# Kernel optimization log

Measured on AMD Instinct MI355X. Metric: run time of the kernel, lower is better.

Reference implementation:

```python
import jax, jax.numpy as jnp
import numpy as np
import math
from jax import lax

B, C, BINS, W = 2, 8, 1024, 512
HEADS = 8
HD = BINS // HEADS            # 128 head dim
ROT = HD // 2                 # rotary rot_dim = bins//num_heads//2 = 64


def setup_inputs() -> dict:
    key = jax.random.key(0)
    k1, k2, k3, k4, k5 = jax.random.split(key, 5)
    s_lin = 1.0 / math.sqrt(BINS)
    return {
        "x": jax.random.normal(k1, (B, C, BINS, W), dtype=jnp.float32),
        "Wq_lin": jax.random.uniform(k2, (C, BINS, BINS), jnp.float32, -s_lin, s_lin),
        "Wq_conv": jax.random.normal(k3, (C, C, 1, 3), dtype=jnp.float32) * 0.1,
        "bq_conv": jax.random.normal(k4, (C,), dtype=jnp.float32) * 0.1,
        "Wout": jax.random.uniform(k5, (C, BINS, BINS), jnp.float32, -s_lin, s_lin),
    }


def _mc_linear(x, Wc):
    # separable MultichannelLinear: out[b,c,o,w] = sum_i W[c,o,i] x[b,c,i,w]
    return jnp.einsum('coi,bciw->bcow', Wc, x)


def _proj(x, Wl, Wc, bc):
    y = _mc_linear(x, Wl)
    y = lax.conv_general_dilated(y, Wc, (1, 1), ((0, 0), (1, 1)),
                                 dimension_numbers=('NCHW', 'OIHW', 'NCHW'))
    return y + bc[None, :, None, None]


def _to_heads(y):
    # [b,c,bins,w] -> [b,c,H,w,hd]
    b, c, _, w = y.shape
    return y.transpose(0, 1, 3, 2).reshape(b, c, w, HEADS, HD).transpose(0, 1, 3, 2, 4)


def _rotary(t):
    # lucidrains RotaryEmbedding(dim=ROT, freqs_for='lang'): rotate first ROT dims over seq axis (-2)
    inv = 1.0 / (10000.0 ** (jnp.arange(0, ROT, 2, dtype=jnp.float32) / ROT))  # [ROT//2]
    pos = jnp.arange(t.shape[-2], dtype=jnp.float32)
    f = jnp.repeat(pos[:, None] * inv[None, :], 2, axis=-1)  # [w, ROT] interleaved repeat
    cos, sin = jnp.cos(f), jnp.sin(f)
    left, right = t[..., :ROT], t[..., ROT:]
    x1, x2 = left[..., 0::2], left[..., 1::2]
    rot = jnp.stack([-x2, x1], axis=-1).reshape(left.shape)
    return jnp.concatenate([left * cos + rot * sin, right], axis=-1)


def reference(x, Wq_lin, Wq_conv, bq_conv, Wout):
    b, c, h, w = x.shape
    # NOTE: original forward uses q_proj for q, k AND v (k_proj/v_proj unused)
    qp = _proj(x, Wq_lin, Wq_conv, bq_conv)
    qh = _to_heads(qp)                       # [b,c,H,w,hd]
    q = _rotary(qh)
    k = _rotary(qh)
    v = qh
    scale = 1.0 / math.sqrt(h)               # custom scale: sqrt(bins), not sqrt(head_dim)
    qk = jnp.einsum('bchqd,bchkd->bchqk', q, k) * scale
    a = jnp.einsum('bchqk,bchkd->bchqd', jax.nn.softmax(qk, axis=-1), v)
    # [b,c,H,w,hd] -> [b,c,bins,w]
    a = a.transpose(0, 1, 3, 2, 4).reshape(b, c, w, h).transpose(0, 1, 3, 2)
    return _mc_linear(a, Wout)
```

## Files before the change

kernel.cpp:

```cpp
#include <hip/hip_runtime.h>
#include <cstddef>

#define Bb 2
#define Cc_ 8
#define BINS 1024
#define Ww 512
#define HEADS 8
#define HD 128
#define NELEM (Bb*Cc_*BINS*Ww)

typedef __attribute__((ext_vector_type(8)))  __bf16 bf16x8;
typedef __attribute__((ext_vector_type(4)))  __bf16 bf16x4;
typedef __attribute__((ext_vector_type(4)))  float  f32x4;
typedef __attribute__((ext_vector_type(16))) float  f32x16;
#define MFMA32(a,b,c) __builtin_amdgcn_mfma_f32_32x32x16_bf16(a,b,c,0,0,0)

__device__ __forceinline__ void async16(const __bf16* g, __bf16* l) {
    __builtin_amdgcn_global_load_lds(
        (const __attribute__((address_space(1))) void*)g,
        (__attribute__((address_space(3))) void*)l, 16, 0, 0);
}

__global__ void __launch_bounds__(256) cast_bf16_2(const float* __restrict__ inA,
                                                   const float* __restrict__ inB,
                                                   __bf16* __restrict__ outA,
                                                   __bf16* __restrict__ outB) {
    const float* in = blockIdx.y ? inB : inA;
    __bf16* out     = blockIdx.y ? outB : outA;
    size_t i = ((size_t)blockIdx.x * 256 + threadIdx.x) * 8;
    float4 a = *(const float4*)&in[i];
    float4 b = *(const float4*)&in[i + 4];
    bf16x8 o = {(__bf16)a.x, (__bf16)a.y, (__bf16)a.z, (__bf16)a.w,
                (__bf16)b.x, (__bf16)b.y, (__bf16)b.z, (__bf16)b.w};
    *(bf16x8*)&out[i] = o;
}

__global__ void __launch_bounds__(256) transpose_cast_x(const float* __restrict__ x,
                                                        __bf16* __restrict__ xT) {
    int w0 = blockIdx.x * 64, i0 = blockIdx.y * 64, bc = blockIdx.z;
    const float* src = x + (size_t)bc * BINS * Ww;
    __bf16* dst = xT + (size_t)bc * Ww * BINS;
    __shared__ float T[64][65];
    int t = threadIdx.x;
    #pragma unroll
    for (int pass = 0; pass < 4; pass++) {
        int idx = t + pass * 256;
        int il = idx >> 4, ch = idx & 15;
        float4 v = *(const float4*)&src[(size_t)(i0 + il) * Ww + w0 + ch * 4];
        T[il][ch * 4 + 0] = v.x; T[il][ch * 4 + 1] = v.y;
        T[il][ch * 4 + 2] = v.z; T[il][ch * 4 + 3] = v.w;
    }
    __syncthreads();
    #pragma unroll
    for (int pass = 0; pass < 2; pass++) {
        int idx = t + pass * 256;
        int wl = idx >> 3, ch = idx & 7;
        bf16x8 o;
        #pragma unroll
        for (int j = 0; j < 8; j++) o[j] = (__bf16)T[ch * 8 + j][wl];
        *(bf16x8*)&dst[(size_t)(w0 + wl) * BINS + i0 + ch * 8] = o;
    }
}

template<bool BF16OUT>
__global__ void __launch_bounds__(256) gemm32(const __bf16* __restrict__ Wall,
                                              const __bf16* __restrict__ Bt,
                                              void* __restrict__ Yv) {
    int bc = blockIdx.z, c = bc & 7;
    const __bf16* A  = Wall + (size_t)c  * BINS * BINS;
    const __bf16* Bm = Bt   + (size_t)bc * Ww * BINS;
    int n0 = blockIdx.x * 128, m0 = blockIdx.y * 128;

    __shared__ __bf16 Asm[128 * 32];
    __shared__ __bf16 Bsm[128 * 32];

    int t = threadIdx.x, w = t >> 6, l = t & 63;
    int l31 = l & 31, h = l >> 5;
    int wm = w >> 1, wn = w & 1;

    int rowS[2], colS[2];
    #pragma unroll
    for (int j = 0; j < 2; j++) {
        int p = (w * 2 + j) * 64 + l;
        int r = p >> 2, cs = (p & 3) ^ (r & 3);
        rowS[j] = r; colS[j] = cs * 8;
    }

    f32x16 acc[2][2];
    #pragma unroll
    for (int a = 0; a < 2; a++)
        #pragma unroll
        for (int b = 0; b < 2; b++)
            #pragma unroll
            for (int r = 0; r < 16; r++) acc[a][b][r] = 0.f;

    for (int k0 = 0; k0 < BINS; k0 += 32) {
        __syncthreads();
        #pragma unroll
        for (int j = 0; j < 2; j++) {
            async16(A  + (size_t)(m0 + rowS[j]) * BINS + k0 + colS[j],
                    Asm + (w * 2 + j) * 512);
            async16(Bm + (size_t)(n0 + rowS[j]) * BINS + k0 + colS[j],
                    Bsm + (w * 2 + j) * 512);
        }
        __syncthreads();
        bf16x8 af[2][2], bfr[2][2];
        #pragma unroll
        for (int mt = 0; mt < 2; mt++)
            #pragma unroll
            for (int kc = 0; kc < 2; kc++) {
                int row = wm * 64 + mt * 32 + l31;
                int ch = (kc * 2 + h) ^ (row & 3);
                af[mt][kc] = *(bf16x8*)&Asm[row * 32 + ch * 8];
            }
        #pragma unroll
        for (int nt = 0; nt < 2; nt++)
            #pragma unroll
            for (int kc = 0; kc < 2; kc++) {
                int row = wn * 64 + nt * 32 + l31;
                int ch = (kc * 2 + h) ^ (row & 3);
                bfr[nt][kc] = *(bf16x8*)&Bsm[row * 32 + ch * 8];
            }
        #pragma unroll
        for (int kc = 0; kc < 2; kc++)
            #pragma unroll
            for (int mt = 0; mt < 2; mt++)
                #pragma unroll
                for (int nt = 0; nt < 2; nt++)
                    acc[mt][nt] = MFMA32(af[mt][kc], bfr[nt][kc], acc[mt][nt]);
    }

    #pragma unroll
    for (int mt = 0; mt < 2; mt++)
        #pragma unroll
        for (int nt = 0; nt < 2; nt++)
            #pragma unroll
            for (int reg = 0; reg < 16; reg++) {
                int m = m0 + wm * 64 + mt * 32 + (reg & 3) + 8 * (reg >> 2) + 4 * h;
                int n = n0 + wn * 64 + nt * 32 + l31;
                if constexpr (BF16OUT) {
                    __bf16* Cm = (__bf16*)Yv + (size_t)bc * BINS * Ww;
                    Cm[(size_t)m * Ww + n] = (__bf16)acc[mt][nt][reg];
                } else {
                    float* Cm = (float*)Yv + (size_t)bc * BINS * Ww;
                    Cm[(size_t)m * Ww + n] = acc[mt][nt][reg];
                }
            }
}

__global__ void __launch_bounds__(256) conv1x3_reg(const __bf16* __restrict__ y,
                                                   const float* __restrict__ Wc,
                                                   const float* __restrict__ bias,
                                                   __bf16* __restrict__ vt) {
    int tid = blockIdx.x * 256 + threadIdx.x;
    int wc = tid & 63;
    int h  = (tid >> 6) & 1023;
    int b  = tid >> 16;
    int w0 = wc * 8;

    float ym[8][8], yl[8], yr[8];
    #pragma unroll
    for (int ci = 0; ci < 8; ci++) {
        const __bf16* row = y + ((size_t)(b * 8 + ci) * BINS + h) * Ww;
        bf16x8 v = *(const bf16x8*)&row[w0];
        #pragma unroll
        for (int j = 0; j < 8; j++) ym[ci][j] = (float)v[j];
        yl[ci] = (w0 > 0)   ? (float)row[w0 - 1] : 0.f;
        yr[ci] = (w0 < 504) ? (float)row[w0 + 8] : 0.f;
    }
    #pragma unroll
    for (int co = 0; co < 8; co++) {
        float acc[8];
        float bv = bias[co];
        #pragma unroll
        for (int j = 0; j < 8; j++) acc[j] = bv;
        #pragma unroll
        for (int ci = 0; ci < 8; ci++) {
            float wa = Wc[(co * 8 + ci) * 3 + 0];
            float wb = Wc[(co * 8 + ci) * 3 + 1];
            float wcc = Wc[(co * 8 + ci) * 3 + 2];
            acc[0] += yl[ci] * wa;
            #pragma unroll
            for (int j = 1; j < 8; j++) acc[j] += ym[ci][j - 1] * wa;
            #pragma unroll
            for (int j = 0; j < 8; j++) acc[j] += ym[ci][j] * wb;
            #pragma unroll
            for (int j = 0; j < 7; j++) acc[j] += ym[ci][j + 1] * wcc;
            acc[7] += yr[ci] * wcc;
        }
        bf16x8 o;
        #pragma unroll
        for (int j = 0; j < 8; j++) o[j] = (__bf16)acc[j];
        *(bf16x8*)&vt[((size_t)(b * 8 + co) * BINS + h) * Ww + w0] = o;
    }
}

__global__ void __launch_bounds__(256) rotary_transpose(const __bf16* __restrict__ vt,
                                                        __bf16* __restrict__ qrot) {
    int p0  = blockIdx.x * 64;
    int bch = blockIdx.y;
    int t = threadIdx.x;
    __shared__ float T[64 * 129];

    const __bf16* src = vt + (size_t)bch * HD * Ww;
    for (int pass = 0; pass < 4; pass++) {
        int idx = t + pass * 256;
        int d = idx >> 3, ch = idx & 7;
        bf16x8 v = *(const bf16x8*)&src[(size_t)d * Ww + p0 + ch * 8];
        #pragma unroll
        for (int j = 0; j < 8; j++) T[(ch * 8 + j) * 129 + d] = (float)v[j];
    }
    __syncthreads();
    for (int pass = 0; pass < 4; pass++) {
        int idx = t + pass * 256;
        int p = idx >> 4, chunk = idx & 15;
        float pos = (float)(p0 + p);
        bf16x8 o;
        if (chunk < 8) {
            #pragma unroll
            for (int j = 0; j < 8; j += 2) {
                int d = chunk * 8 + j;
                int jj = d >> 1;
                float inv = __expf(-(2.0f * jj / 64.0f) * 9.210340371976184f);
                float sn, cs;
                __sincosf(pos * inv, &sn, &cs);
                float x1 = T[p * 129 + d];
                float x2 = T[p * 129 + d + 1];
                o[j]     = (__bf16)(x1 * cs - x2 * sn);
                o[j + 1] = (__bf16)(x2 * cs + x1 * sn);
            }
        } else {
            #pragma unroll
            for (int j = 0; j < 8; j++)
                o[j] = (__bf16)T[p * 129 + chunk * 8 + j];
        }
        *(bf16x8*)&qrot[((size_t)bch * Ww + p0 + p) * HD + chunk * 8] = o;
    }
}

__global__ void __launch_bounds__(256, 2) attn32(const __bf16* __restrict__ qrot,
                                                 const __bf16* __restrict__ vt,
                                                 __bf16* __restrict__ attnT) {
    int bid = blockIdx.x;
    int bch = bid & 127, q0 = (bid >> 7) * 128;
    int t = threadIdx.x, wv = t >> 6, lane = t & 63;
    int l31 = lane & 31, h = lane >> 5;

    __shared__ __align__(16) char smem[49152];
    __bf16* Ks  = (__bf16*)smem;
    __bf16* Vts = (__bf16*)(smem + 16384);
    __bf16* Psw = (__bf16*)(smem + 32768) + wv * 2048;

    const __bf16* qb = qrot + (size_t)bch * Ww * HD;
    const __bf16* vb = vt   + (size_t)bch * HD * Ww;

    int qrow = q0 + wv * 32 + l31;
    bf16x8 qf[8];
    #pragma unroll
    for (int c = 0; c < 8; c++) {
        bf16x8 v = *(const bf16x8*)&qb[(size_t)qrow * HD + c * 16 + h * 8];
        #pragma unroll
        for (int j = 0; j < 8; j++) v[j] = (__bf16)((float)v[j] * 0.03125f);
        qf[c] = v;
    }

    f32x16 oacc[4];
    #pragma unroll
    for (int dt = 0; dt < 4; dt++)
        #pragma unroll
        for (int r = 0; r < 16; r++) oacc[dt][r] = 0.f;
    float m_st = -1e30f, l_st = 0.f;

    for (int kt = 0; kt < 8; kt++) {
        int k0 = kt * 64;
        __syncthreads();
        #pragma unroll
        for (int i = 0; i < 4; i++) {
            int p = wv * 256 + i * 64 + lane;
            int r  = p >> 4, cs  = ((p & 15) ^ (r & 15)) * 8;
            async16(qb + (size_t)(k0 + r) * HD + cs, Ks + (wv * 256 + i * 64) * 8);
            int r2 = p >> 3, cs2 = ((p & 7) ^ (r2 & 7)) * 8;
            async16(vb + (size_t)r2 * Ww + k0 + cs2, Vts + (wv * 256 + i * 64) * 8);
        }
        __syncthreads();

        f32x16 st[2];
        #pragma unroll
        for (int t2 = 0; t2 < 2; t2++)
            #pragma unroll
            for (int r = 0; r < 16; r++) st[t2][r] = 0.f;
        #pragma unroll
        for (int c = 0; c < 8; c++)
            #pragma unroll
            for (int t2 = 0; t2 < 2; t2++) {
                int row = t2 * 32 + l31;
                int ch = (c * 2 + h) ^ (row & 15);
                bf16x8 ak = *(bf16x8*)&Ks[row * 128 + ch * 8];
                st[t2] = MFMA32(ak, qf[c], st[t2]);
            }

        float mx = -1e30f;
        #pragma unroll
        for (int t2 = 0; t2 < 2; t2++)
            #pragma unroll
            for (int r = 0; r < 16; r++) mx = fmaxf(mx, st[t2][r]);
        mx = fmaxf(mx, __shfl_xor(mx, 32));
        float mnew = fmaxf(m_st, mx);
        float alpha = __expf(m_st - mnew);
        float sum = 0.f;
        #pragma unroll
        for (int t2 = 0; t2 < 2; t2++)
            #pragma unroll
            for (int r = 0; r < 16; r++) {
                float p = __expf(st[t2][r] - mnew);
                st[t2][r] = p;
                sum += p;
            }
        sum += __shfl_xor(sum, 32);
        l_st = l_st * alpha + sum;
        m_st = mnew;

        #pragma unroll
        for (int t2 = 0; t2 < 2; t2++)
            #pragma unroll
            for (int g = 0; g < 4; g++) {
                bf16x4 pk = {(__bf16)st[t2][4 * g],     (__bf16)st[t2][4 * g + 1],
                             (__bf16)st[t2][4 * g + 2], (__bf16)st[t2][4 * g + 3]};
                int ch = (t2 * 4 + g) ^ (l31 & 7);
                *(bf16x4*)&Psw[l31 * 64 + ch * 8 + 4 * h] = pk;
            }
        #pragma unroll
        for (int dt = 0; dt < 4; dt++)
            #pragma unroll
            for (int r = 0; r < 16; r++) oacc[dt][r] *= alpha;

        #pragma unroll
        for (int kc = 0; kc < 4; kc++) {
            int chp = (kc * 2 + h) ^ (l31 & 7);
            bf16x8 bp = *(bf16x8*)&Psw[l31 * 64 + chp * 8];
            #pragma unroll
            for (int dt = 0; dt < 4; dt++) {
                int row = dt * 32 + l31;
                int cv = (kc * 2 + h) ^ (row & 7);
                bf16x8 av = *(bf16x8*)&Vts[row * 64 + cv * 8];
                oacc[dt] = MFMA32(av, bp, oacc[dt]);
            }
        }
    }

    __syncthreads();
    __bf16* Ob = (__bf16*)smem + wv * 4096;
    float linv = 1.f / l_st;
    #pragma unroll
    for (int dt = 0; dt < 4; dt++)
        #pragma unroll
        for (int g = 0; g < 4; g++) {
            bf16x4 pk = {(__bf16)(oacc[dt][4 * g] * linv),
                         (__bf16)(oacc[dt][4 * g + 1] * linv),
                         (__bf16)(oacc[dt][4 * g + 2] * linv),
                         (__bf16)(oacc[dt][4 * g + 3] * linv)};
            int ch = (dt * 4 + g) ^ (l31 & 15);
            *(bf16x4*)&Ob[l31 * 128 + ch * 8 + 4 * h] = pk;
        }
    int bc = bch >> 3, h0 = bch & 7;
    #pragma unroll
    for (int i = 0; i < 8; i++) {
        int p = i * 64 + lane;
        int rr = p >> 4, cc = p & 15;
        int cs = cc ^ (rr & 15);
        bf16x8 v = *(bf16x8*)&Ob[rr * 128 + cs * 8];
        *(bf16x8*)&attnT[((size_t)bc * Ww + q0 + wv * 32 + rr) * BINS + h0 * HD + cc * 8] = v;
    }
}

extern "C" void kernel_launch(void* const* d_in, const int* in_sizes, int n_in,
                              void* d_out, int out_size, void* d_ws, size_t ws_size,
                              hipStream_t stream) {
    const float* x       = (const float*)d_in[0];
    const float* Wq_lin  = (const float*)d_in[1];
    const float* Wq_conv = (const float*)d_in[2];
    const float* bq_conv = (const float*)d_in[3];
    const float* Wout    = (const float*)d_in[4];
    float* out = (float*)d_out;

    __bf16* U = (__bf16*)d_ws;
    __bf16* Wq_bf   = U;
    __bf16* xT      = U + 1 * (size_t)NELEM;
    __bf16* Wout_bf = U + 2 * (size_t)NELEM;
    __bf16* y       = U + 3 * (size_t)NELEM;
    __bf16* vtb     = U + 4 * (size_t)NELEM;
    __bf16* qrot    = U + 5 * (size_t)NELEM;
    __bf16* attnT   = U + 3 * (size_t)NELEM;

    cast_bf16_2<<<dim3(NELEM / (8 * 256), 2), 256, 0, stream>>>(Wq_lin, Wout, Wq_bf, Wout_bf);
    transpose_cast_x<<<dim3(Ww / 64, BINS / 64, Bb * Cc_), 256, 0, stream>>>(x, xT);
    gemm32<true><<<dim3(Ww / 128, BINS / 128, Bb * Cc_), 256, 0, stream>>>(Wq_bf, xT, y);
    conv1x3_reg<<<dim3(Bb * BINS * 64 / 256), 256, 0, stream>>>(y, Wq_conv, bq_conv, vtb);
    rotary_transpose<<<dim3(Ww / 64, Bb * Cc_ * HEADS), 256, 0, stream>>>(vtb, qrot);
    attn32<<<dim3((Ww / 128) * 128), 256, 0, stream>>>(qrot, vtb, attnT);
    gemm32<false><<<dim3(Ww / 128, BINS / 128, Bb * Cc_), 256, 0, stream>>>(Wout_bf, attnT, out);
}
```

Measured before the change: 253.0 us.

## Merge prep kernels, deepen GEMM K-tile, stage GEMM epilogue through LDS

Folds the two weight-cast launches and the x transpose-cast into one prep kernel to save a launch. The GEMM K step doubles from 32 to 64, with an 8-way XOR swizzle and twice the LDS, so there are half as many barrier round trips per tile. The epilogue now writes accumulators to LDS and then stores coalesced 16-byte rows instead of scattered scalar stores, at the cost of extra barriers and higher LDS use that may lower occupancy.

Result: faster. 236.5 us (-6.5%).

```diff
diff --git a/kernel.cpp b/kernel.cpp
--- a/kernel.cpp
+++ b/kernel.cpp
@@ -21,27 +21,32 @@
         (__attribute__((address_space(3))) void*)l, 16, 0, 0);
 }
 
-__global__ void __launch_bounds__(256) cast_bf16_2(const float* __restrict__ inA,
-                                                   const float* __restrict__ inB,
-                                                   __bf16* __restrict__ outA,
-                                                   __bf16* __restrict__ outB) {
-    const float* in = blockIdx.y ? inB : inA;
-    __bf16* out     = blockIdx.y ? outB : outA;
-    size_t i = ((size_t)blockIdx.x * 256 + threadIdx.x) * 8;
-    float4 a = *(const float4*)&in[i];
-    float4 b = *(const float4*)&in[i + 4];
-    bf16x8 o = {(__bf16)a.x, (__bf16)a.y, (__bf16)a.z, (__bf16)a.w,
-                (__bf16)b.x, (__bf16)b.y, (__bf16)b.z, (__bf16)b.w};
-    *(bf16x8*)&out[i] = o;
-}
-
-__global__ void __launch_bounds__(256) transpose_cast_x(const float* __restrict__ x,
-                                                        __bf16* __restrict__ xT) {
-    int w0 = blockIdx.x * 64, i0 = blockIdx.y * 64, bc = blockIdx.z;
+__global__ void __launch_bounds__(256) prep(const float* __restrict__ Wq,
+                                            const float* __restrict__ Wout,
+                                            const float* __restrict__ x,
+                                            __bf16* __restrict__ Wqb,
+                                            __bf16* __restrict__ Woutb,
+                                            __bf16* __restrict__ xT) {
+    int bid = blockIdx.x;
+    int t = threadIdx.x;
+    if (bid < 8192) {
+        const float* in = (bid < 4096) ? Wq : Wout;
+        __bf16* out     = (bid < 4096) ? Wqb : Woutb;
+        size_t i = ((size_t)(bid & 4095) * 256 + t) * 8;
+        float4 a = *(const float4*)&in[i];
+        float4 b = *(const float4*)&in[i + 4];
+        bf16x8 o = {(__bf16)a.x, (__bf16)a.y, (__bf16)a.z, (__bf16)a.w,
+                    (__bf16)b.x, (__bf16)b.y, (__bf16)b.z, (__bf16)b.w};
+        *(bf16x8*)&out[i] = o;
+        return;
+    }
+    int b2 = bid - 8192;
+    int w0 = (b2 & 7) * 64;
+    int i0 = ((b2 >> 3) & 15) * 64;
+    int bc = b2 >> 7;
     const float* src = x + (size_t)bc * BINS * Ww;
     __bf16* dst = xT + (size_t)bc * Ww * BINS;
     __shared__ float T[64][65];
-    int t = threadIdx.x;
     #pragma unroll
     for (int pass = 0; pass < 4; pass++) {
         int idx = t + pass * 256;
@@ -71,18 +76,19 @@
     const __bf16* Bm = Bt   + (size_t)bc * Ww * BINS;
     int n0 = blockIdx.x * 128, m0 = blockIdx.y * 128;
 
-    __shared__ __bf16 Asm[128 * 32];
-    __shared__ __bf16 Bsm[128 * 32];
+    __shared__ __align__(16) char smem[32768];
+    __bf16* Asm = (__bf16*)smem;
+    __bf16* Bsm = (__bf16*)(smem + 16384);
 
     int t = threadIdx.x, w = t >> 6, l = t & 63;
     int l31 = l & 31, h = l >> 5;
     int wm = w >> 1, wn = w & 1;
 
-    int rowS[2], colS[2];
-    #pragma unroll
-    for (int j = 0; j < 2; j++) {
-        int p = (w * 2 + j) * 64 + l;
-        int r = p >> 2, cs = (p & 3) ^ (r & 3);
+    int rowS[4], colS[4];
+    #pragma unroll
+    for (int j = 0; j < 4; j++) {
+        int p = j * 256 + w * 64 + l;
+        int r = p >> 3, cs = (p & 7) ^ (r & 7);
         rowS[j] = r; colS[j] = cs * 8;
     }
 
@@ -94,35 +100,35 @@
             #pragma unroll
             for (int r = 0; r < 16; r++) acc[a][b][r] = 0.f;
 
-    for (int k0 = 0; k0 < BINS; k0 += 32) {
+    for (int k0 = 0; k0 < BINS; k0 += 64) {
         __syncthreads();
         #pragma unroll
-        for (int j = 0; j < 2; j++) {
+        for (int j = 0; j < 4; j++) {
             async16(A  + (size_t)(m0 + rowS[j]) * BINS + k0 + colS[j],
-                    Asm + (w * 2 + j) * 512);
+                    Asm + (j * 256 + w * 64) * 8);
             async16(Bm + (size_t)(n0 + rowS[j]) * BINS + k0 + colS[j],
-                    Bsm + (w * 2 + j) * 512);
+                    Bsm + (j * 256 + w * 64) * 8);
         }
         __syncthreads();
-        bf16x8 af[2][2], bfr[2][2];
+        bf16x8 af[2][4], bfr[2][4];
         #pragma unroll
         for (int mt = 0; mt < 2; mt++)
             #pragma unroll
-            for (int kc = 0; kc < 2; kc++) {
+            for (int kc = 0; kc < 4; kc++) {
                 int row = wm * 64 + mt * 32 + l31;
-                int ch = (kc * 2 + h) ^ (row & 3);
-                af[mt][kc] = *(bf16x8*)&Asm[row * 32 + ch * 8];
+                int ch = (kc * 2 + h) ^ (row & 7);
+                af[mt][kc] = *(bf16x8*)&Asm[row * 64 + ch * 8];
             }
         #pragma unroll
         for (int nt = 0; nt < 2; nt++)
             #pragma unroll
-            for (int kc = 0; kc < 2; kc++) {
+            for (int kc = 0; kc < 4; kc++) {
                 int row = wn * 64 + nt * 32 + l31;
-                int ch = (kc * 2 + h) ^ (row & 3);
-                bfr[nt][kc] = *(bf16x8*)&Bsm[row * 32 + ch * 8];
-            }
-        #pragma unroll
-        for (int kc = 0; kc < 2; kc++)
+                int ch = (kc * 2 + h) ^ (row & 7);
+                bfr[nt][kc] = *(bf16x8*)&Bsm[row * 64 + ch * 8];
+            }
+        #pragma unroll
+        for (int kc = 0; kc < 4; kc++)
             #pragma unroll
             for (int mt = 0; mt < 2; mt++)
                 #pragma unroll
@@ -130,22 +136,56 @@
                     acc[mt][nt] = MFMA32(af[mt][kc], bfr[nt][kc], acc[mt][nt]);
     }
 
-    #pragma unroll
-    for (int mt = 0; mt < 2; mt++)
-        #pragma unroll
-        for (int nt = 0; nt < 2; nt++)
-            #pragma unroll
-            for (int reg = 0; reg < 16; reg++) {
-                int m = m0 + wm * 64 + mt * 32 + (reg & 3) + 8 * (reg >> 2) + 4 * h;
-                int n = n0 + wn * 64 + nt * 32 + l31;
-                if constexpr (BF16OUT) {
-                    __bf16* Cm = (__bf16*)Yv + (size_t)bc * BINS * Ww;
-                    Cm[(size_t)m * Ww + n] = (__bf16)acc[mt][nt][reg];
-                } else {
-                    float* Cm = (float*)Yv + (size_t)bc * BINS * Ww;
-                    Cm[(size_t)m * Ww + n] = acc[mt][nt][reg];
+    __syncthreads();
+    if constexpr (BF16OUT) {
+        __bf16* Ob = (__bf16*)smem;
+        __bf16* Cm = (__bf16*)Yv + (size_t)bc * BINS * Ww;
+        #pragma unroll
+        for (int mt = 0; mt < 2; mt++)
+            #pragma unroll
+            for (int nt = 0; nt < 2; nt++)
+                #pragma unroll
+                for (int reg = 0; reg < 16; reg++) {
+                    int ml = wm * 64 + mt * 32 + (reg & 3) + 8 * (reg >> 2) + 4 * h;
+                    int nl = wn * 64 + nt * 32 + l31;
+                    Ob[ml * 128 + nl] = (__bf16)acc[mt][nt][reg];
                 }
-            }
+        __syncthreads();
+        #pragma unroll
+        for (int pass = 0; pass < 8; pass++) {
+            int idx = t + pass * 256;
+            int row = idx >> 4, ch = idx & 15;
+            *(bf16x8*)&Cm[(size_t)(m0 + row) * Ww + n0 + ch * 8] =
+                *(bf16x8*)&Ob[row * 128 + ch * 8];
+        }
+    } else {
+        float* Of = (float*)smem;
+        float* Cm = (float*)Yv + (size_t)bc * BINS * Ww;
+        #pragma unroll
+        for (int half = 0; half < 2; half++) {
+            if (wm == half) {
+                #pragma unroll
+                for (int mt = 0; mt < 2; mt++)
+                    #pragma unroll
+                    for (int nt = 0; nt < 2; nt++)
+                        #pragma unroll
+                        for (int reg = 0; reg < 16; reg++) {
+                            int ml = mt * 32 + (reg & 3) + 8 * (reg >> 2) + 4 * h;
+                            int nl = wn * 64 + nt * 32 + l31;
+                            Of[ml * 128 + nl] = acc[mt][nt][reg];
+                        }
+            }
+            __syncthreads();
+            #pragma unroll
+            for (int pass = 0; pass < 8; pass++) {
+                int idx = t + pass * 256;
+                int row = idx >> 5, c4 = idx & 31;
+                *(float4*)&Cm[(size_t)(m0 + half * 64 + row) * Ww + n0 + c4 * 4] =
+                    *(float4*)&Of[row * 128 + c4 * 4];
+            }
+            __syncthreads();
+        }
+    }
 }
 
 __global__ void __launch_bounds__(256) conv1x3_reg(const __bf16* __restrict__ y,
@@ -392,8 +432,7 @@
     __bf16* qrot    = U + 5 * (size_t)NELEM;
     __bf16* attnT   = U + 3 * (size_t)NELEM;
 
-    cast_bf16_2<<<dim3(NELEM / (8 * 256), 2), 256, 0, stream>>>(Wq_lin, Wout, Wq_bf, Wout_bf);
-    transpose_cast_x<<<dim3(Ww / 64, BINS / 64, Bb * Cc_), 256, 0, stream>>>(x, xT);
+    prep<<<dim3(8192 + 2048), 256, 0, stream>>>(Wq_lin, Wout, x, Wq_bf, Wout_bf, xT);
     gemm32<true><<<dim3(Ww / 128, BINS / 128, Bb * Cc_), 256, 0, stream>>>(Wq_bf, xT, y);
     conv1x3_reg<<<dim3(Bb * BINS * 64 / 256), 256, 0, stream>>>(y, Wq_conv, bq_conv, vtb);
     rotary_transpose<<<dim3(Ww / 64, Bb * Cc_ * HEADS), 256, 0, stream>>>(vtb, qrot);
```
